# Kernel optimization log

Measured on AMD Instinct MI355X. Metric: run time of the kernel, lower is better.

## Reference

```python
import jax, jax.numpy as jnp
import numpy as np

LORA_RANK = 16
LORA_ALPHA = 32
CHUNK_SIZE = 256
TTT_LR = 0.01
CLIP_THRESHOLD = 1.0
SCALING = LORA_ALPHA / LORA_RANK
LN_EPS = 1e-5


def setup_inputs() -> dict:
    key = jax.random.key(0)
    ks = jax.random.split(key, 5)
    B, S, K, H = 2, 8192, 1024, 1024
    x = jax.random.normal(ks[0], (B, S, K), dtype=jnp.float32)
    Wb = jax.random.normal(ks[1], (H, K), dtype=jnp.float32) / np.sqrt(K)
    init_A = jax.random.normal(ks[2], (H, LORA_RANK), dtype=jnp.float32) * 0.01
    init_B = jax.random.normal(ks[3], (LORA_RANK, K), dtype=jnp.float32) * 0.01
    ln_gamma = jnp.ones((K,), dtype=jnp.float32)
    ln_beta = jnp.zeros((K,), dtype=jnp.float32)
    Wp = jax.random.normal(ks[4], (H, K), dtype=jnp.float32) / np.sqrt(K)
    return {"x": x, "Wb": Wb, "init_A": init_A, "init_B": init_B,
            "ln_gamma": ln_gamma, "ln_beta": ln_beta, "Wp": Wp}


def _forward(x, Wb, init_A, init_B, ln_gamma, ln_beta, Wp):
    B_sz, Seq, k_dim = x.shape
    h_dim = Wb.shape[0]
    r = init_A.shape[1]
    nc = Seq // CHUNK_SIZE  # Seq chosen divisible; pad_len == 0

    base_out = x @ Wb.T  # [B, S, H]

    # --- target construction under no_grad: LayerNorm + left-shift ---
    xd = jax.lax.stop_gradient(x)
    mu = jnp.mean(xd, axis=-1, keepdims=True)
    var = jnp.mean((xd - mu) ** 2, axis=-1, keepdims=True)
    xn = (xd - mu) * jax.lax.rsqrt(var + LN_EPS) * ln_gamma + ln_beta
    shifted = jnp.pad(xn[:, 1:, :], ((0, 0), (0, 1), (0, 0)))
    shifted = jax.lax.stop_gradient(shifted)

    V = shifted @ Wp.T  # [B, S, H]

    Z = x.reshape(B_sz * nc, CHUNK_SIZE, k_dim)
    Vc = V.reshape(B_sz * nc, CHUNK_SIZE, h_dim)

    # per-chunk fast-weight deltas
    proj_in = Z @ init_B.T                                # [BC, C, r]
    dA = jnp.einsum('bch,bcr->bhr', Vc, proj_in)          # [BC, H, r]
    proj_err = Vc @ init_A                                # [BC, C, r]
    dB = jnp.einsum('bcr,bck->brk', proj_err, Z)          # [BC, r, K]

    dA = dA.reshape(B_sz, nc, h_dim, r)
    dB = dB.reshape(B_sz, nc, r, k_dim)

    # exclusive cross-chunk cumsum
    accA = jnp.cumsum(dA, axis=1)
    accB = jnp.cumsum(dB, axis=1)
    accA = jnp.concatenate([jnp.zeros_like(accA[:, :1]), accA[:, :-1]], axis=1)
    accB = jnp.concatenate([jnp.zeros_like(accB[:, :1]), accB[:, :-1]], axis=1)

    lr = TTT_LR * SCALING
    rawA = (lr * accA).reshape(-1, h_dim, r)
    rawB = (lr * accB).reshape(-1, r, k_dim)

    # joint norm clip (norm_type=2)
    norm_sq = (jnp.sum(rawA.astype(jnp.float32) ** 2, axis=(-2, -1), keepdims=True)
               + jnp.sum(rawB.astype(jnp.float32) ** 2, axis=(-2, -1), keepdims=True))
    total_norm = jnp.sqrt(norm_sq)
    coef = jnp.minimum(CLIP_THRESHOLD / (total_norm + 1e-6), 1.0).astype(rawA.dtype)

    A_eff = init_A[None] - rawA * coef  # [BC, H, r]
    B_eff = init_B[None] - rawB * coef  # [BC, r, K]

    mid = jnp.einsum('bck,brk->bcr', Z, B_eff)          # [BC, C, r]
    lora = jnp.einsum('bcr,bhr->bch', mid, A_eff)       # [BC, C, H]
    lora = lora.reshape(B_sz, Seq, h_dim)

    return base_out + lora * SCALING


def reference(x, Wb, init_A, init_B, ln_gamma, ln_beta, Wp):
    return _forward(x, Wb, init_A, init_B, ln_gamma, ln_beta, Wp)
```

## Files before the change

### kernel.cpp

```cpp
#include <hip/hip_runtime.h>

typedef __attribute__((ext_vector_type(8))) short s16x8;
typedef __attribute__((ext_vector_type(4))) float f32x4;
typedef unsigned short u16;

#define B_SZ 2
#define SEQ 8192
#define KD 1024
#define HD 1024
#define RK 16
#define CH 256
#define NCH 64
static constexpr float LR_SC = 0.02f;
static constexpr float SCALE_OUT = 2.0f;

__device__ __forceinline__ u16 f2b(float f) {
  union { float f; unsigned int u; } c; c.f = f;
  unsigned int u = c.u;
  unsigned int r = (u + 0x7fffu + ((u >> 16) & 1u)) >> 16;
  return (u16)r;
}
__device__ __forceinline__ float b2f(u16 v) {
  union { unsigned int u; float f; } c; c.u = ((unsigned int)v) << 16; return c.f;
}
__device__ __forceinline__ void async16(const u16* g, u16* l) {
  __builtin_amdgcn_global_load_lds((const __attribute__((address_space(1))) void*)g,
                                   (__attribute__((address_space(3))) void*)l, 16, 0, 0);
}

__global__ __launch_bounds__(256) void cvt_all(const float* __restrict__ Wb,
                                               const float* __restrict__ Wp,
                                               const float* __restrict__ initB,
                                               u16* __restrict__ Wbb,
                                               u16* __restrict__ Wpb,
                                               u16* __restrict__ iBb) {
  int bid = blockIdx.x;
  const float* src; u16* dst; int base;
  if (bid < 1024)      { src = Wb;    dst = Wbb; base = bid; }
  else if (bid < 2048) { src = Wp;    dst = Wpb; base = bid - 1024; }
  else                 { src = initB; dst = iBb; base = bid - 2048; }
  int i = (base * 256 + threadIdx.x) * 4;
  float4 v = *(const float4*)(src + i);
  ushort4 o; o.x = f2b(v.x); o.y = f2b(v.y); o.z = f2b(v.z); o.w = f2b(v.w);
  *(ushort4*)(dst + i) = o;
}

__global__ __launch_bounds__(256) void wpat_part(const float* __restrict__ initA,
                                                 const float* __restrict__ Wp,
                                                 float* __restrict__ part) {
  int t = threadIdx.x;
  int k = blockIdx.x * 256 + t;
  int hseg = blockIdx.y;
  __shared__ float Asm[256 * 16];
  for (int i = t; i < 1024; i += 256)
    *(float4*)&Asm[i * 4] = *(const float4*)&initA[(size_t)hseg * 4096 + i * 4];
  __syncthreads();
  float acc[16];
  #pragma unroll
  for (int j = 0; j < 16; j++) acc[j] = 0.f;
  const float* wp = Wp + (size_t)hseg * 256 * KD + k;
  #pragma unroll 4
  for (int hh = 0; hh < 256; hh++) {
    float w = wp[(size_t)hh * KD];
    const float4* ar = (const float4*)&Asm[hh * 16];
    #pragma unroll
    for (int q = 0; q < 4; q++) {
      float4 a = ar[q];
      acc[q*4+0] += w * a.x; acc[q*4+1] += w * a.y;
      acc[q*4+2] += w * a.z; acc[q*4+3] += w * a.w;
    }
  }
  float* o = part + ((size_t)hseg * 1024 + k) * 16;
  #pragma unroll
  for (int q = 0; q < 4; q++) {
    float4 r; r.x = acc[q*4]; r.y = acc[q*4+1]; r.z = acc[q*4+2]; r.w = acc[q*4+3];
    *(float4*)&o[q * 4] = r;
  }
}

__global__ __launch_bounds__(256) void wpat_reduce(const float* __restrict__ part,
                                                   u16* __restrict__ WpAT) {
  int idx = blockIdx.x * 256 + threadIdx.x;
  int k = idx & 1023, r = idx >> 10;
  float s = part[((size_t)0 * 1024 + k) * 16 + r]
          + part[((size_t)1 * 1024 + k) * 16 + r]
          + part[((size_t)2 * 1024 + k) * 16 + r]
          + part[((size_t)3 * 1024 + k) * 16 + r];
  WpAT[(size_t)r * KD + k] = f2b(s);
}

__global__ __launch_bounds__(256) void ln_shift(const float* __restrict__ x,
                                                const float* __restrict__ gamma,
                                                const float* __restrict__ beta,
                                                u16* __restrict__ xb,
                                                u16* __restrict__ shb) {
  int row = blockIdx.x;
  int t = threadIdx.x;
  int s = row & (SEQ - 1);
  const float* xr = x + (size_t)row * KD;
  float4 v = *(const float4*)(xr + t * 4);
  ushort4 o; o.x = f2b(v.x); o.y = f2b(v.y); o.z = f2b(v.z); o.w = f2b(v.w);
  *(ushort4*)(xb + (size_t)row * KD + t * 4) = o;

  if (s == 0) {
    ushort4 z; z.x = 0; z.y = 0; z.z = 0; z.w = 0;
    *(ushort4*)(shb + ((size_t)row + SEQ - 1) * KD + t * 4) = z;
    return;
  }
  float s1 = v.x + v.y + v.z + v.w;
  float s2 = v.x * v.x + v.y * v.y + v.z * v.z + v.w * v.w;
  #pragma unroll
  for (int off = 32; off > 0; off >>= 1) {
    s1 += __shfl_down(s1, off);
    s2 += __shfl_down(s2, off);
  }
  __shared__ float red[8];
  int wave = t >> 6, lane = t & 63;
  if (lane == 0) { red[wave * 2] = s1; red[wave * 2 + 1] = s2; }
  __syncthreads();
  float sum = red[0] + red[2] + red[4] + red[6];
  float ssq = red[1] + red[3] + red[5] + red[7];
  float mu = sum * (1.0f / KD);
  float var = ssq * (1.0f / KD) - mu * mu;
  float rstd = rsqrtf(var + 1e-5f);
  float4 g = *(const float4*)(gamma + t * 4);
  float4 bb = *(const float4*)(beta + t * 4);
  ushort4 so;
  so.x = f2b((v.x - mu) * rstd * g.x + bb.x);
  so.y = f2b((v.y - mu) * rstd * g.y + bb.y);
  so.z = f2b((v.z - mu) * rstd * g.z + bb.z);
  so.w = f2b((v.w - mu) * rstd * g.w + bb.w);
  *(ushort4*)(shb + (size_t)(row - 1) * KD + t * 4) = so;
}

__global__ __launch_bounds__(256, 2) void gemm_fused(const u16* __restrict__ A,
                                                     const u16* __restrict__ Bm,
                                                     const u16* __restrict__ mid2,
                                                     const u16* __restrict__ Aef,
                                                     float* __restrict__ C) {
  constexpr int BM = 128, BN = 128, BK = 64, N = HD, Kd = KD;
  __shared__ u16 As[BM * BK];
  __shared__ u16 Bs[BN * BK];
  int tid = threadIdx.x;
  int lane = tid & 63, wave = tid >> 6;
  int lb = blockIdx.x + 8 * blockIdx.y;
  int q = lb & 7, t = lb >> 3;
  int mb = q * 16 + (t >> 3);
  int nb = t & 7;
  int m0 = mb * 128, n0 = nb * 128;
  int wm = (wave >> 1) * 64, wn = (wave & 1) * 64;
  int lr = lane & 15;
  int qd = lane >> 4;
  int sw = lr & 7;
  int slot0 = ((qd ^ sw) * 8);
  int slot1 = (((4 + qd) ^ sw) * 8);
  f32x4 acc[4][4] = {};

  const u16* gbase; u16* lbase;
  if (wave < 2) { gbase = A + (size_t)(m0 + wave * 64) * Kd; lbase = As + wave * 64 * BK; }
  else          { gbase = Bm + (size_t)(n0 + (wave - 2) * 64) * Kd; lbase = Bs + (wave - 2) * 64 * BK; }
  int srow = lane >> 3;
  int scol = ((lane & 7) ^ srow) * 8;
  const u16* gsrc = gbase + (size_t)srow * Kd + scol;

  for (int k0 = 0; k0 < Kd; k0 += BK) {
    #pragma unroll
    for (int i = 0; i < 8; i++)
      async16(gsrc + (size_t)i * 8 * Kd, lbase + i * 512);
    gsrc += BK;
    __syncthreads();
    s16x8 af[4], bfr[4];
    #pragma unroll
    for (int i = 0; i < 4; i++) af[i] = *(const s16x8*)(As + (wm + i * 16 + lr) * BK + slot0);
    #pragma unroll
    for (int j = 0; j < 4; j++) bfr[j] = *(const s16x8*)(Bs + (wn + j * 16 + lr) * BK + slot0);
    #pragma unroll
    for (int i = 0; i < 4; i++)
      #pragma unroll
      for (int j = 0; j < 4; j++)
        acc[i][j] = __builtin_amdgcn_mfma_f32_16x16x32_bf16(af[i], bfr[j], acc[i][j], 0, 0, 0);
    #pragma unroll
    for (int i = 0; i < 4; i++) af[i] = *(const s16x8*)(As + (wm + i * 16 + lr) * BK + slot1);
    #pragma unroll
    for (int j = 0; j < 4; j++) bfr[j] = *(const s16x8*)(Bs + (wn + j * 16 + lr) * BK + slot1);
    #pragma unroll
    for (int i = 0; i < 4; i++)
      #pragma unroll
      for (int j = 0; j < 4; j++)
        acc[i][j] = __builtin_amdgcn_mfma_f32_16x16x32_bf16(af[i], bfr[j], acc[i][j], 0, 0, 0);
    __syncthreads();
  }

  {
    int chunk = m0 >> 8;
    const u16* abase = Aef + (size_t)chunk * (HD * RK);
    int klane = lane >> 4;
    s16x8 am2[4], bn2[4];
    #pragma unroll
    for (int i = 0; i < 4; i++) {
      if (klane < 2)
        am2[i] = *(const s16x8*)(mid2 + (size_t)(m0 + wm + i * 16 + lr) * RK + klane * 8);
      else { s16x8 z = {}; am2[i] = z; }
    }
    #pragma unroll
    for (int j = 0; j < 4; j++) {
      if (klane < 2)
        bn2[j] = *(const s16x8*)(abase + (size_t)(n0 + wn + j * 16 + lr) * RK + klane * 8);
      else { s16x8 z = {}; bn2[j] = z; }
    }
    #pragma unroll
    for (int i = 0; i < 4; i++)
      #pragma unroll
      for (int j = 0; j < 4; j++)
        acc[i][j] = __builtin_amdgcn_mfma_f32_16x16x32_bf16(am2[i], bn2[j], acc[i][j], 0, 0, 0);
  }

  int rb = (lane >> 4) * 4, cc = lane & 15;
  #pragma unroll
  for (int i = 0; i < 4; i++)
    #pragma unroll
    for (int j = 0; j < 4; j++)
      #pragma unroll
      for (int p = 0; p < 4; p++)
        C[(size_t)(m0 + wm + i * 16 + rb + p) * N + (n0 + wn + j * 16 + cc)] = acc[i][j][p];
}

__global__ __launch_bounds__(256) void rank16_proj(const u16* __restrict__ xb,
                                                   const u16* __restrict__ shb,
                                                   const u16* __restrict__ iBb,
                                                   const u16* __restrict__ WpAT,
                                                   float* __restrict__ pin,
                                                   float* __restrict__ per) {
  const u16* X; const u16* W; float* O;
  if (blockIdx.z == 0) { X = xb; W = iBb; O = pin; }
  else                 { X = shb; W = WpAT; O = per; }
  int wave = threadIdx.x >> 6, lane = threadIdx.x & 63;
  int m0 = (blockIdx.x * 4 + wave) * 16;
  int lr = lane & 15, lk = (lane >> 4) * 8;
  const u16* xp = X + (size_t)(m0 + lr) * KD + lk;
  const u16* wp = W + (size_t)lr * KD + lk;
  f32x4 acc = {};
  #pragma unroll 4
  for (int k0 = 0; k0 < KD; k0 += 32) {
    s16x8 a = *(const s16x8*)xp;
    s16x8 b = *(const s16x8*)wp;
    acc = __builtin_amdgcn_mfma_f32_16x16x32_bf16(a, b, acc, 0, 0, 0);
    xp += 32; wp += 32;
  }
  int rb = (lane >> 4) * 4, cc = lane & 15;
  #pragma unroll
  for (int p = 0; p < 4; p++)
    O[(size_t)(m0 + rb + p) * RK + cc] = acc[p];
}

__global__ __launch_bounds__(256) void rank16_mid(const u16* __restrict__ xb,
                                                  const u16* __restrict__ Bef,
                                                  u16* __restrict__ mid2) {
  int wave = threadIdx.x >> 6, lane = threadIdx.x & 63;
  int m0 = (blockIdx.x * 4 + wave) * 16;
  int chunk = m0 >> 8;
  int lr = lane & 15, lk = (lane >> 4) * 8;
  const u16* xp = xb + (size_t)(m0 + lr) * KD + lk;
  const u16* wp = Bef + (size_t)chunk * (RK * KD) + (size_t)lr * KD + lk;
  f32x4 acc = {};
  #pragma unroll 4
  for (int k0 = 0; k0 < KD; k0 += 32) {
    s16x8 a = *(const s16x8*)xp;
    s16x8 b = *(const s16x8*)wp;
    acc = __builtin_amdgcn_mfma_f32_16x16x32_bf16(a, b, acc, 0, 0, 0);
    xp += 32; wp += 32;
  }
  int rb = (lane >> 4) * 4, cc = lane & 15;
  #pragma unroll
  for (int p = 0; p < 4; p++)
    mid2[(size_t)(m0 + rb + p) * RK + cc] = f2b(SCALE_OUT * acc[p]);
}

__global__ __launch_bounds__(256) void gk_kernel(const u16* __restrict__ xb,
                                                 const u16* __restrict__ shb,
                                                 const float* __restrict__ pin,
                                                 const float* __restrict__ per,
                                                 float* __restrict__ G,
                                                 float* __restrict__ dB) {
  int tile = blockIdx.x;
  int chunk = blockIdx.y;
  int which = blockIdx.z;
  int t = threadIdx.x;
  __shared__ float P[CH * RK];
  const float* psrc = which ? per : pin;
  for (int i = t; i < 1024; i += 256)
    *(float4*)&P[i * 4] = *(const float4*)&psrc[(size_t)chunk * 4096 + i * 4];
  __syncthreads();
  float acc[16];
  #pragma unroll
  for (int j = 0; j < 16; j++) acc[j] = 0.f;
  int col = tile * 256 + t;
  const u16* src = (which ? xb : shb) + (size_t)chunk * CH * KD + col;
  for (int c = 0; c < 256; c++) {
    float v = b2f(src[(size_t)c * 1024]);
    const float4* pr = (const float4*)&P[c * 16];
    #pragma unroll
    for (int q = 0; q < 4; q++) {
      float4 p = pr[q];
      acc[q*4+0] += v * p.x; acc[q*4+1] += v * p.y;
      acc[q*4+2] += v * p.z; acc[q*4+3] += v * p.w;
    }
  }
  float* o = (which ? dB : G) + (size_t)chunk * 16384 + col;
  #pragma unroll
  for (int j = 0; j < 16; j++) o[(size_t)j * 1024] = acc[j];
}

__global__ __launch_bounds__(256) void cumsum_kernel(const float* __restrict__ G,
                                                     const float* __restrict__ dB,
                                                     u16* __restrict__ rawG,
                                                     float* __restrict__ rawB) {
  int idx = blockIdx.x * 256 + threadIdx.x;
  int which = idx >> 15;
  int rem = idx & 32767;
  int b = rem >> 14;
  int e = rem & 16383;
  size_t base = (size_t)b * 32 * 16384 + e;
  if (which == 0) {
    float run = 0.f;
    for (int i = 0; i < 32; i++) {
      size_t off = base + (size_t)i * 16384;
      float nv = G[off];
      rawG[off] = f2b(LR_SC * run);
      run += nv;
    }
  } else {
    float run = 0.f;
    for (int i = 0; i < 32; i++) {
      size_t off = base + (size_t)i * 16384;
      float nv = dB[off];
      rawB[off] = LR_SC * run;
      run += nv;
    }
  }
}

__global__ __launch_bounds__(256) void dagemm(const u16* __restrict__ Wpb,
                                              const u16* __restrict__ rawG,
                                              float* __restrict__ rawA) {
  int wave = threadIdx.x >> 6, lane = threadIdx.x & 63;
  int m0 = (blockIdx.x * 4 + wave) * 16;
  int chunk = blockIdx.y;
  int lr = lane & 15, lk = (lane >> 4) * 8;
  const u16* ap = Wpb + (size_t)(m0 + lr) * KD + lk;
  const u16* bp = rawG + (size_t)chunk * 16384 + (size_t)lr * KD + lk;
  f32x4 acc = {};
  #pragma unroll 4
  for (int k0 = 0; k0 < KD; k0 += 32) {
    s16x8 a = *(const s16x8*)ap;
    s16x8 b = *(const s16x8*)bp;
    acc = __builtin_amdgcn_mfma_f32_16x16x32_bf16(a, b, acc, 0, 0, 0);
    ap += 32; bp += 32;
  }
  int rb = (lane >> 4) * 4, cc = lane & 15;
  #pragma unroll
  for (int p = 0; p < 4; p++)
    rawA[(size_t)chunk * 16384 + (size_t)(m0 + rb + p) * RK + cc] = acc[p];
}

__global__ __launch_bounds__(256) void coef_eff(const float* __restrict__ initA,
                                                const float* __restrict__ initB,
                                                const float* __restrict__ rawA,
                                                const float* __restrict__ rawB,
                                                u16* __restrict__ Aef,
                                                u16* __restrict__ Bef) {
  int chunk = blockIdx.x, t = threadIdx.x;
  const float* a = rawA + (size_t)chunk * 16384;
  const float* b = rawB + (size_t)chunk * 16384;
  float s = 0.f;
  for (int i = t * 4; i < 16384; i += 1024) {
    float4 v = *(const float4*)(a + i);
    s += v.x*v.x + v.y*v.y + v.z*v.z + v.w*v.w;
    float4 w = *(const float4*)(b + i);
    s += w.x*w.x + w.y*w.y + w.z*w.z + w.w*w.w;
  }
  #pragma unroll
  for (int off = 32; off > 0; off >>= 1) s += __shfl_down(s, off);
  __shared__ float red[4];
  int wave = t >> 6, lane = t & 63;
  if (lane == 0) red[wave] = s;
  __syncthreads();
  float tot = red[0] + red[1] + red[2] + red[3];
  float cf = fminf(1.0f / (sqrtf(tot) + 1e-6f), 1.0f);
  u16* ao = Aef + (size_t)chunk * 16384;
  u16* bo = Bef + (size_t)chunk * 16384;
  for (int i = t * 4; i < 16384; i += 1024) {
    float4 iv = *(const float4*)(initA + i);
    float4 rv = *(const float4*)(a + i);
    ushort4 r;
    r.x = f2b(iv.x - rv.x * cf); r.y = f2b(iv.y - rv.y * cf);
    r.z = f2b(iv.z - rv.z * cf); r.w = f2b(iv.w - rv.w * cf);
    *(ushort4*)(ao + i) = r;
    float4 iw = *(const float4*)(initB + i);
    float4 rw = *(const float4*)(b + i);
    ushort4 rr;
    rr.x = f2b(iw.x - rw.x * cf); rr.y = f2b(iw.y - rw.y * cf);
    rr.z = f2b(iw.z - rw.z * cf); rr.w = f2b(iw.w - rw.w * cf);
    *(ushort4*)(bo + i) = rr;
  }
}

extern "C" void kernel_launch(void* const* d_in, const int* in_sizes, int n_in,
                              void* d_out, int out_size, void* d_ws, size_t ws_size,
                              hipStream_t stream) {
  (void)in_sizes; (void)n_in; (void)out_size; (void)ws_size;
  const float* x     = (const float*)d_in[0];
  const float* Wb    = (const float*)d_in[1];
  const float* initA = (const float*)d_in[2];
  const float* initB = (const float*)d_in[3];
  const float* gamma = (const float*)d_in[4];
  const float* beta  = (const float*)d_in[5];
  const float* Wp    = (const float*)d_in[6];
  float* out = (float*)d_out;

  char* ws = (char*)d_ws;
  size_t off = 0;
  auto alloc = [&](size_t bytes) -> void* {
    void* p = ws + off;
    off = (off + bytes + 255) & ~(size_t)255;
    return p;
  };
  const size_t ROWS = (size_t)B_SZ * SEQ;
  u16* xb    = (u16*)alloc(ROWS * KD * 2);
  u16* shb   = (u16*)alloc(ROWS * KD * 2);
  u16* Wbb   = (u16*)alloc((size_t)HD * KD * 2);
  u16* Wpb   = (u16*)alloc((size_t)HD * KD * 2);
  u16* iBb   = (u16*)alloc((size_t)RK * KD * 2);
  u16* WpAT  = (u16*)alloc((size_t)RK * KD * 2);
  float* wpart = (float*)alloc((size_t)4 * KD * RK * 4);
  float* pin = (float*)alloc((size_t)NCH * CH * RK * 4);
  float* per = (float*)alloc((size_t)NCH * CH * RK * 4);
  float* G   = (float*)alloc((size_t)NCH * 16384 * 4);
  float* dB  = (float*)alloc((size_t)NCH * 16384 * 4);
  u16* rawG  = (u16*)alloc((size_t)NCH * 16384 * 2);
  float* rawB= (float*)alloc((size_t)NCH * 16384 * 4);
  float* rawA= (float*)alloc((size_t)NCH * 16384 * 4);
  u16* Aef   = (u16*)alloc((size_t)NCH * 16384 * 2);
  u16* Bef   = (u16*)alloc((size_t)NCH * 16384 * 2);
  u16* mid2  = (u16*)alloc(ROWS * RK * 2);

  cvt_all<<<2064, 256, 0, stream>>>(Wb, Wp, initB, Wbb, Wpb, iBb);
  wpat_part<<<dim3(4, 4), 256, 0, stream>>>(initA, Wp, wpart);
  wpat_reduce<<<64, 256, 0, stream>>>(wpart, WpAT);
  ln_shift<<<ROWS, 256, 0, stream>>>(x, gamma, beta, xb, shb);
  rank16_proj<<<dim3(256, 1, 2), 256, 0, stream>>>(xb, shb, iBb, WpAT, pin, per);
  gk_kernel<<<dim3(4, NCH, 2), 256, 0, stream>>>(xb, shb, pin, per, G, dB);
  cumsum_kernel<<<256, 256, 0, stream>>>(G, dB, rawG, rawB);
  dagemm<<<dim3(16, NCH), 256, 0, stream>>>(Wpb, rawG, rawA);
  coef_eff<<<NCH, 256, 0, stream>>>(initA, initB, rawA, rawB, Aef, Bef);
  rank16_mid<<<256, 256, 0, stream>>>(xb, Bef, mid2);
  gemm_fused<<<dim3(8, 128), 256, 0, stream>>>(xb, Wbb, mid2, Aef, out);
}
```

Measured before the change: 313.0 us.

## Fuse rank-16 mid projection into main GEMM and widen small prep kernels

Removes the separate rank16_mid kernel. The mid = x·B_effᵀ product is now computed inside gemm_fused's K-loop from the A tile already in LDS, then written to shared memory for the LoRA epilogue. This drops one launch and a second full pass over xb, at the cost of extra MFMAs and global Bef loads in every GEMM block; each n-tile also recomputes mid redundantly. Separately, wpat_part is split into 16 h-segments instead of 4 for more parallelism, and coef_eff now uses 1024 threads per block.

```diff
diff --git a/kernel.cpp b/kernel.cpp
--- a/kernel.cpp
+++ b/kernel.cpp
@@ -51,30 +51,29 @@
   int t = threadIdx.x;
   int k = blockIdx.x * 256 + t;
   int hseg = blockIdx.y;
-  __shared__ float Asm[256 * 16];
-  for (int i = t; i < 1024; i += 256)
-    *(float4*)&Asm[i * 4] = *(const float4*)&initA[(size_t)hseg * 4096 + i * 4];
+  __shared__ float Asm[64 * 16];
+  *(float4*)&Asm[t * 4] = *(const float4*)&initA[(size_t)hseg * 1024 + t * 4];
   __syncthreads();
   float acc[16];
   #pragma unroll
   for (int j = 0; j < 16; j++) acc[j] = 0.f;
-  const float* wp = Wp + (size_t)hseg * 256 * KD + k;
-  #pragma unroll 4
-  for (int hh = 0; hh < 256; hh++) {
+  const float* wp = Wp + (size_t)hseg * 64 * KD + k;
+  #pragma unroll 8
+  for (int hh = 0; hh < 64; hh++) {
     float w = wp[(size_t)hh * KD];
     const float4* ar = (const float4*)&Asm[hh * 16];
     #pragma unroll
-    for (int q = 0; q < 4; q++) {
-      float4 a = ar[q];
-      acc[q*4+0] += w * a.x; acc[q*4+1] += w * a.y;
-      acc[q*4+2] += w * a.z; acc[q*4+3] += w * a.w;
+    for (int qq = 0; qq < 4; qq++) {
+      float4 a = ar[qq];
+      acc[qq*4+0] += w * a.x; acc[qq*4+1] += w * a.y;
+      acc[qq*4+2] += w * a.z; acc[qq*4+3] += w * a.w;
     }
   }
   float* o = part + ((size_t)hseg * 1024 + k) * 16;
   #pragma unroll
-  for (int q = 0; q < 4; q++) {
-    float4 r; r.x = acc[q*4]; r.y = acc[q*4+1]; r.z = acc[q*4+2]; r.w = acc[q*4+3];
-    *(float4*)&o[q * 4] = r;
+  for (int qq = 0; qq < 4; qq++) {
+    float4 r; r.x = acc[qq*4]; r.y = acc[qq*4+1]; r.z = acc[qq*4+2]; r.w = acc[qq*4+3];
+    *(float4*)&o[qq * 4] = r;
   }
 }
 
@@ -82,10 +81,10 @@
                                                    u16* __restrict__ WpAT) {
   int idx = blockIdx.x * 256 + threadIdx.x;
   int k = idx & 1023, r = idx >> 10;
-  float s = part[((size_t)0 * 1024 + k) * 16 + r]
-          + part[((size_t)1 * 1024 + k) * 16 + r]
-          + part[((size_t)2 * 1024 + k) * 16 + r]
-          + part[((size_t)3 * 1024 + k) * 16 + r];
+  float s = 0.f;
+  #pragma unroll
+  for (int seg = 0; seg < 16; seg++)
+    s += part[((size_t)seg * 1024 + k) * 16 + r];
   WpAT[(size_t)r * KD + k] = f2b(s);
 }
 
@@ -135,7 +134,7 @@
 
 __global__ __launch_bounds__(256, 2) void gemm_fused(const u16* __restrict__ A,
                                                      const u16* __restrict__ Bm,
-                                                     const u16* __restrict__ mid2,
+                                                     const u16* __restrict__ Bef,
                                                      const u16* __restrict__ Aef,
                                                      float* __restrict__ C) {
   constexpr int BM = 128, BN = 128, BK = 64, N = HD, Kd = KD;
@@ -148,13 +147,17 @@
   int mb = q * 16 + (t >> 3);
   int nb = t & 7;
   int m0 = mb * 128, n0 = nb * 128;
+  int chunk = m0 >> 8;
   int wm = (wave >> 1) * 64, wn = (wave & 1) * 64;
+  int wm2 = wave * 32;
   int lr = lane & 15;
   int qd = lane >> 4;
   int sw = lr & 7;
   int slot0 = ((qd ^ sw) * 8);
   int slot1 = (((4 + qd) ^ sw) * 8);
+  int rb = qd * 4, cc = lr;
   f32x4 acc[4][4] = {};
+  f32x4 macc[2] = {};
 
   const u16* gbase; u16* lbase;
   if (wave < 2) { gbase = A + (size_t)(m0 + wave * 64) * Kd; lbase = As + wave * 64 * BK; }
@@ -162,6 +165,7 @@
   int srow = lane >> 3;
   int scol = ((lane & 7) ^ srow) * 8;
   const u16* gsrc = gbase + (size_t)srow * Kd + scol;
+  const u16* befk = Bef + (size_t)chunk * (RK * KD) + (size_t)lr * Kd + qd * 8;
 
   for (int k0 = 0; k0 < Kd; k0 += BK) {
     #pragma unroll
@@ -188,18 +192,36 @@
       #pragma unroll
       for (int j = 0; j < 4; j++)
         acc[i][j] = __builtin_amdgcn_mfma_f32_16x16x32_bf16(af[i], bfr[j], acc[i][j], 0, 0, 0);
+    {
+      s16x8 bf0 = *(const s16x8*)(befk);
+      s16x8 bf1 = *(const s16x8*)(befk + 32);
+      #pragma unroll
+      for (int i2 = 0; i2 < 2; i2++) {
+        s16x8 a0 = *(const s16x8*)(As + (wm2 + i2 * 16 + lr) * BK + slot0);
+        macc[i2] = __builtin_amdgcn_mfma_f32_16x16x32_bf16(a0, bf0, macc[i2], 0, 0, 0);
+        s16x8 a1 = *(const s16x8*)(As + (wm2 + i2 * 16 + lr) * BK + slot1);
+        macc[i2] = __builtin_amdgcn_mfma_f32_16x16x32_bf16(a1, bf1, macc[i2], 0, 0, 0);
+      }
+      befk += BK;
+    }
     __syncthreads();
   }
 
+  #pragma unroll
+  for (int i2 = 0; i2 < 2; i2++)
+    #pragma unroll
+    for (int p = 0; p < 4; p++)
+      As[(wm2 + i2 * 16 + rb + p) * 16 + cc] = f2b(SCALE_OUT * macc[i2][p]);
+  __syncthreads();
+
   {
-    int chunk = m0 >> 8;
     const u16* abase = Aef + (size_t)chunk * (HD * RK);
     int klane = lane >> 4;
     s16x8 am2[4], bn2[4];
     #pragma unroll
     for (int i = 0; i < 4; i++) {
       if (klane < 2)
-        am2[i] = *(const s16x8*)(mid2 + (size_t)(m0 + wm + i * 16 + lr) * RK + klane * 8);
+        am2[i] = *(const s16x8*)(As + (wm + i * 16 + lr) * 16 + klane * 8);
       else { s16x8 z = {}; am2[i] = z; }
     }
     #pragma unroll
@@ -215,7 +237,6 @@
         acc[i][j] = __builtin_amdgcn_mfma_f32_16x16x32_bf16(am2[i], bn2[j], acc[i][j], 0, 0, 0);
   }
 
-  int rb = (lane >> 4) * 4, cc = lane & 15;
   #pragma unroll
   for (int i = 0; i < 4; i++)
     #pragma unroll
@@ -253,29 +274,6 @@
     O[(size_t)(m0 + rb + p) * RK + cc] = acc[p];
 }
 
-__global__ __launch_bounds__(256) void rank16_mid(const u16* __restrict__ xb,
-                                                  const u16* __restrict__ Bef,
-                                                  u16* __restrict__ mid2) {
-  int wave = threadIdx.x >> 6, lane = threadIdx.x & 63;
-  int m0 = (blockIdx.x * 4 + wave) * 16;
-  int chunk = m0 >> 8;
-  int lr = lane & 15, lk = (lane >> 4) * 8;
-  const u16* xp = xb + (size_t)(m0 + lr) * KD + lk;
-  const u16* wp = Bef + (size_t)chunk * (RK * KD) + (size_t)lr * KD + lk;
-  f32x4 acc = {};
-  #pragma unroll 4
-  for (int k0 = 0; k0 < KD; k0 += 32) {
-    s16x8 a = *(const s16x8*)xp;
-    s16x8 b = *(const s16x8*)wp;
-    acc = __builtin_amdgcn_mfma_f32_16x16x32_bf16(a, b, acc, 0, 0, 0);
-    xp += 32; wp += 32;
-  }
-  int rb = (lane >> 4) * 4, cc = lane & 15;
-  #pragma unroll
-  for (int p = 0; p < 4; p++)
-    mid2[(size_t)(m0 + rb + p) * RK + cc] = f2b(SCALE_OUT * acc[p]);
-}
-
 __global__ __launch_bounds__(256) void gk_kernel(const u16* __restrict__ xb,
                                                  const u16* __restrict__ shb,
                                                  const float* __restrict__ pin,
@@ -300,10 +298,10 @@
     float v = b2f(src[(size_t)c * 1024]);
     const float4* pr = (const float4*)&P[c * 16];
     #pragma unroll
-    for (int q = 0; q < 4; q++) {
-      float4 p = pr[q];
-      acc[q*4+0] += v * p.x; acc[q*4+1] += v * p.y;
-      acc[q*4+2] += v * p.z; acc[q*4+3] += v * p.w;
+    for (int qq = 0; qq < 4; qq++) {
+      float4 p = pr[qq];
+      acc[qq*4+0] += v * p.x; acc[qq*4+1] += v * p.y;
+      acc[qq*4+2] += v * p.z; acc[qq*4+3] += v * p.w;
     }
   }
   float* o = (which ? dB : G) + (size_t)chunk * 16384 + col;
@@ -363,17 +361,18 @@
     rawA[(size_t)chunk * 16384 + (size_t)(m0 + rb + p) * RK + cc] = acc[p];
 }
 
-__global__ __launch_bounds__(256) void coef_eff(const float* __restrict__ initA,
-                                                const float* __restrict__ initB,
-                                                const float* __restrict__ rawA,
-                                                const float* __restrict__ rawB,
-                                                u16* __restrict__ Aef,
-                                                u16* __restrict__ Bef) {
+__global__ __launch_bounds__(1024) void coef_eff(const float* __restrict__ initA,
+                                                 const float* __restrict__ initB,
+                                                 const float* __restrict__ rawA,
+                                                 const float* __restrict__ rawB,
+                                                 u16* __restrict__ Aef,
+                                                 u16* __restrict__ Bef) {
   int chunk = blockIdx.x, t = threadIdx.x;
   const float* a = rawA + (size_t)chunk * 16384;
   const float* b = rawB + (size_t)chunk * 16384;
   float s = 0.f;
-  for (int i = t * 4; i < 16384; i += 1024) {
+  #pragma unroll
+  for (int i = t * 4; i < 16384; i += 4096) {
     float4 v = *(const float4*)(a + i);
     s += v.x*v.x + v.y*v.y + v.z*v.z + v.w*v.w;
     float4 w = *(const float4*)(b + i);
@@ -381,15 +380,18 @@
   }
   #pragma unroll
   for (int off = 32; off > 0; off >>= 1) s += __shfl_down(s, off);
-  __shared__ float red[4];
+  __shared__ float red[16];
   int wave = t >> 6, lane = t & 63;
   if (lane == 0) red[wave] = s;
   __syncthreads();
-  float tot = red[0] + red[1] + red[2] + red[3];
+  float tot = 0.f;
+  #pragma unroll
+  for (int w = 0; w < 16; w++) tot += red[w];
   float cf = fminf(1.0f / (sqrtf(tot) + 1e-6f), 1.0f);
   u16* ao = Aef + (size_t)chunk * 16384;
   u16* bo = Bef + (size_t)chunk * 16384;
-  for (int i = t * 4; i < 16384; i += 1024) {
+  #pragma unroll
+  for (int i = t * 4; i < 16384; i += 4096) {
     float4 iv = *(const float4*)(initA + i);
     float4 rv = *(const float4*)(a + i);
     ushort4 r;
@@ -432,7 +434,7 @@
   u16* Wpb   = (u16*)alloc((size_t)HD * KD * 2);
   u16* iBb   = (u16*)alloc((size_t)RK * KD * 2);
   u16* WpAT  = (u16*)alloc((size_t)RK * KD * 2);
-  float* wpart = (float*)alloc((size_t)4 * KD * RK * 4);
+  float* wpart = (float*)alloc((size_t)16 * KD * RK * 4);
   float* pin = (float*)alloc((size_t)NCH * CH * RK * 4);
   float* per = (float*)alloc((size_t)NCH * CH * RK * 4);
   float* G   = (float*)alloc((size_t)NCH * 16384 * 4);
@@ -442,17 +444,15 @@
   float* rawA= (float*)alloc((size_t)NCH * 16384 * 4);
   u16* Aef   = (u16*)alloc((size_t)NCH * 16384 * 2);
   u16* Bef   = (u16*)alloc((size_t)NCH * 16384 * 2);
-  u16* mid2  = (u16*)alloc(ROWS * RK * 2);
 
   cvt_all<<<2064, 256, 0, stream>>>(Wb, Wp, initB, Wbb, Wpb, iBb);
-  wpat_part<<<dim3(4, 4), 256, 0, stream>>>(initA, Wp, wpart);
+  wpat_part<<<dim3(4, 16), 256, 0, stream>>>(initA, Wp, wpart);
   wpat_reduce<<<64, 256, 0, stream>>>(wpart, WpAT);
   ln_shift<<<ROWS, 256, 0, stream>>>(x, gamma, beta, xb, shb);
   rank16_proj<<<dim3(256, 1, 2), 256, 0, stream>>>(xb, shb, iBb, WpAT, pin, per);
   gk_kernel<<<dim3(4, NCH, 2), 256, 0, stream>>>(xb, shb, pin, per, G, dB);
   cumsum_kernel<<<256, 256, 0, stream>>>(G, dB, rawG, rawB);
   dagemm<<<dim3(16, NCH), 256, 0, stream>>>(Wpb, rawG, rawA);
-  coef_eff<<<NCH, 256, 0, stream>>>(initA, initB, rawA, rawB, Aef, Bef);
-  rank16_mid<<<256, 256, 0, stream>>>(xb, Bef, mid2);
-  gemm_fused<<<dim3(8, 128), 256, 0, stream>>>(xb, Wbb, mid2, Aef, out);
-}
+  coef_eff<<<NCH, 1024, 0, stream>>>(initA, initB, rawA, rawB, Aef, Bef);
+  gemm_fused<<<dim3(8, 128), 256, 0, stream>>>(xb, Wbb, Bef, Aef, out);
+}
```

New measurement: 278.6 us. -11.0%, faster.
